# Kernel tuning notes

Measured on AMD Instinct MI355X. Metric: run time of the kernel, lower is better.

## Reference

```python
import jax, jax.numpy as jnp
import numpy as np


def setup_inputs() -> dict:
    key = jax.random.key(0)
    x = jax.random.normal(key, (8, 256, 16384), dtype=jnp.float32)
    gamma = jnp.zeros((1,), dtype=jnp.float32)
    return {"x": x, "gamma": gamma}


def reference(x, gamma):
    # x: (B, C, T)
    # energy[b, i, j] = sum_t x[b, i, t] * x[b, j, t]  -> (B, C, C)
    energy = jnp.einsum('bit,bjt->bij', x, x)
    # max-subtract trick: attention = softmax(max_j(energy) - energy)
    energy_new = jnp.max(energy, axis=-1, keepdims=True) - energy
    attention = jax.nn.softmax(energy_new, axis=-1)
    # out[b, i, t] = sum_j attention[b, i, j] * x[b, j, t]
    out = jnp.einsum('bij,bjt->bit', attention, x)
    return gamma * out + x
```

## Files before the change

### kernel.cpp

```cpp
#include <hip/hip_runtime.h>
#include <hip/hip_bf16.h>

#define NB 8
#define NC 256
#define NT 16384

using bf16x8 = __attribute__((ext_vector_type(8))) __bf16;
using f32x16 = __attribute__((ext_vector_type(16))) float;
using f32x4  = __attribute__((ext_vector_type(4))) float;
using u32x4  = __attribute__((ext_vector_type(4))) unsigned int;

__device__ __forceinline__ unsigned short bf16_rne(float f) {
  unsigned int u = __float_as_uint(f);
  u += 0x7FFFu + ((u >> 16) & 1u);
  return (unsigned short)(u >> 16);
}

__device__ __forceinline__ unsigned int pack_bf16_pair_rne(float f_lo, float f_hi) {
  unsigned int a = __float_as_uint(f_lo), b = __float_as_uint(f_hi);
  a += 0x7FFFu + ((a >> 16) & 1u);
  b += 0x7FFFu + ((b >> 16) & 1u);
  return __builtin_amdgcn_perm(b, a, 0x07060302u);
}

template <int ITERS>
__global__ __launch_bounds__(1024) void k_gram(const float* __restrict__ x,
                                               float* __restrict__ Gp) {
  __shared__ __align__(16) unsigned short lds[256 * 72];
  const int b   = blockIdx.y;
  const int kc  = blockIdx.x;
  const int tid = threadIdx.x;
  const int l   = tid & 63, w = tid >> 6;
  const int wr  = w >> 2, wc = w & 3;
  const int l31 = l & 31, lh = l >> 5;

  const float* __restrict__ xb = x + (size_t)b * NC * NT;

  const int sr = tid >> 2;
  const int sq = tid & 3;
  const float* sp = xb + (size_t)sr * NT + kc * (ITERS * 64) + sq * 16;

  f32x4 r0 = ((const f32x4*)sp)[0];
  f32x4 r1 = ((const f32x4*)sp)[1];
  f32x4 r2 = ((const f32x4*)sp)[2];
  f32x4 r3 = ((const f32x4*)sp)[3];

  f32x16 acc00, acc01, acc10, acc11;
#pragma unroll
  for (int i = 0; i < 16; ++i) { acc00[i] = 0.f; acc01[i] = 0.f; acc10[i] = 0.f; acc11[i] = 0.f; }

#pragma unroll 1
  for (int it = 0; it < ITERS; ++it) {
    __syncthreads();
    u32x4 p0, p1;
    p0[0] = pack_bf16_pair_rne(r0[0], r0[1]); p0[1] = pack_bf16_pair_rne(r0[2], r0[3]);
    p0[2] = pack_bf16_pair_rne(r1[0], r1[1]); p0[3] = pack_bf16_pair_rne(r1[2], r1[3]);
    p1[0] = pack_bf16_pair_rne(r2[0], r2[1]); p1[1] = pack_bf16_pair_rne(r2[2], r2[3]);
    p1[2] = pack_bf16_pair_rne(r3[0], r3[1]); p1[3] = pack_bf16_pair_rne(r3[2], r3[3]);
    u32x4* dst = (u32x4*)&lds[sr * 72 + sq * 16];
    dst[0] = p0;
    dst[1] = p1;
    if (it < ITERS - 1) {
      const float* np = sp + (it + 1) * 64;
      r0 = ((const f32x4*)np)[0]; r1 = ((const f32x4*)np)[1];
      r2 = ((const f32x4*)np)[2]; r3 = ((const f32x4*)np)[3];
    }
    __syncthreads();
#pragma unroll
    for (int s = 0; s < 4; ++s) {
      const int ko = s * 16 + lh * 8;
      bf16x8 a0 = *(const bf16x8*)&lds[(wr * 64 +      l31) * 72 + ko];
      bf16x8 a1 = *(const bf16x8*)&lds[(wr * 64 + 32 + l31) * 72 + ko];
      bf16x8 b0 = *(const bf16x8*)&lds[(wc * 64 +      l31) * 72 + ko];
      bf16x8 b1 = *(const bf16x8*)&lds[(wc * 64 + 32 + l31) * 72 + ko];
      acc00 = __builtin_amdgcn_mfma_f32_32x32x16_bf16(a0, b0, acc00, 0, 0, 0);
      acc01 = __builtin_amdgcn_mfma_f32_32x32x16_bf16(a0, b1, acc01, 0, 0, 0);
      acc10 = __builtin_amdgcn_mfma_f32_32x32x16_bf16(a1, b0, acc10, 0, 0, 0);
      acc11 = __builtin_amdgcn_mfma_f32_32x32x16_bf16(a1, b1, acc11, 0, 0, 0);
    }
  }

  float* __restrict__ Gb = Gp + ((size_t)kc * NB + b) * NC * NC;
  const int ibase = wr * 64 + 4 * lh;
  const int jbase = wc * 64 + l31;
#pragma unroll
  for (int g = 0; g < 16; ++g) {
    const int ir = (g & 3) + 8 * (g >> 2);
    Gb[(ibase + ir) * NC      + jbase     ] = acc00[g];
    Gb[(ibase + ir) * NC      + jbase + 32] = acc01[g];
    Gb[(ibase + 32 + ir) * NC + jbase     ] = acc10[g];
    Gb[(ibase + 32 + ir) * NC + jbase + 32] = acc11[g];
  }
}

template <int NKC>
__global__ __launch_bounds__(256) void k_softmax(const float* __restrict__ Gp,
                                                 const float* __restrict__ gamma,
                                                 unsigned short* __restrict__ Att) {
  const int row = blockIdx.x * 4 + (threadIdx.x >> 6);
  const int l   = threadIdx.x & 63;
  const int i   = row & (NC - 1);
  const float* base = Gp + (size_t)row * NC + l * 4;

  f32x4 v; v[0] = 0.f; v[1] = 0.f; v[2] = 0.f; v[3] = 0.f;
#pragma unroll
  for (int kc = 0; kc < NKC; ++kc) {
    f32x4 p = *(const f32x4*)(base + (size_t)kc * (NB * NC * NC));
    v[0] += p[0]; v[1] += p[1]; v[2] += p[2]; v[3] += p[3];
  }

  float mn = fminf(fminf(v[0], v[1]), fminf(v[2], v[3]));
#pragma unroll
  for (int m = 32; m >= 1; m >>= 1) mn = fminf(mn, __shfl_xor(mn, m, 64));
  float p0 = __expf(mn - v[0]), p1 = __expf(mn - v[1]);
  float p2 = __expf(mn - v[2]), p3 = __expf(mn - v[3]);
  float s = (p0 + p1) + (p2 + p3);
#pragma unroll
  for (int m = 32; m >= 1; m >>= 1) s += __shfl_xor(s, m, 64);
  const float sc = gamma[0] / s;

  const int j0 = 4 * l;
  ushort4 o;
  o.x = bf16_rne(p0 * sc + ((j0 + 0) == i ? 1.f : 0.f));
  o.y = bf16_rne(p1 * sc + ((j0 + 1) == i ? 1.f : 0.f));
  o.z = bf16_rne(p2 * sc + ((j0 + 2) == i ? 1.f : 0.f));
  o.w = bf16_rne(p3 * sc + ((j0 + 3) == i ? 1.f : 0.f));
  *(ushort4*)(Att + (size_t)row * NC + j0) = o;
}

__global__ __launch_bounds__(1024) void k_out(const float* __restrict__ x,
                                              const unsigned short* __restrict__ Att,
                                              float* __restrict__ y) {
  __shared__ __align__(16) float bs[32 * 260];
  __shared__ __align__(16) unsigned short as_[256 * 40];
  const int b   = blockIdx.y;
  const int t0  = blockIdx.x * 256;
  const int tid = threadIdx.x;
  const int l   = tid & 63, w = tid >> 6;
  const int rbw = w >> 3, cbw = w & 7;
  const int l31 = l & 31, lh = l >> 5;

  const float* __restrict__ xb = x + (size_t)b * NC * NT;
  const unsigned short* __restrict__ Ab = Att + (size_t)b * NC * NC;

  const int bk = tid >> 5, bf = tid & 31;
  const int ar = tid >> 2, aseg = tid & 3;

  const float* bsp = xb + (size_t)bk * NT + t0 + bf * 4;
  f32x4 rb0 = *(const f32x4*)bsp;
  f32x4 rb1 = *(const f32x4*)(bsp + 128);
  u32x4 ra  = *(const u32x4*)(Ab + ar * NC + aseg * 8);

  f32x16 acc0, acc1, acc2, acc3;
#pragma unroll
  for (int i = 0; i < 16; ++i) { acc0[i] = 0.f; acc1[i] = 0.f; acc2[i] = 0.f; acc3[i] = 0.f; }

#pragma unroll 1
  for (int it = 0; it < 8; ++it) {
    __syncthreads();
    *(f32x4*)&bs[bk * 260 + bf * 4]       = rb0;
    *(f32x4*)&bs[bk * 260 + 128 + bf * 4] = rb1;
    *(u32x4*)&as_[ar * 40 + aseg * 8]     = ra;
    if (it < 7) {
      const float* np = bsp + (size_t)(it + 1) * 32 * NT;
      rb0 = *(const f32x4*)np;
      rb1 = *(const f32x4*)(np + 128);
      ra  = *(const u32x4*)(Ab + ar * NC + (it + 1) * 32 + aseg * 8);
    }
    __syncthreads();
#pragma unroll
    for (int s = 0; s < 2; ++s) {
      const int kr = s * 16 + lh * 8;
      const int tc = cbw * 32 + l31;
      float f0 = bs[(kr + 0) * 260 + tc], f1 = bs[(kr + 1) * 260 + tc];
      float f2 = bs[(kr + 2) * 260 + tc], f3 = bs[(kr + 3) * 260 + tc];
      float f4 = bs[(kr + 4) * 260 + tc], f5 = bs[(kr + 5) * 260 + tc];
      float f6 = bs[(kr + 6) * 260 + tc], f7 = bs[(kr + 7) * 260 + tc];
      u32x4 pk;
      pk[0] = pack_bf16_pair_rne(f0, f1); pk[1] = pack_bf16_pair_rne(f2, f3);
      pk[2] = pack_bf16_pair_rne(f4, f5); pk[3] = pack_bf16_pair_rne(f6, f7);
      bf16x8 bfrag = __builtin_bit_cast(bf16x8, pk);
      const int ao = s * 16 + lh * 8;
      bf16x8 a0 = *(const bf16x8*)&as_[(rbw * 128 +      l31) * 40 + ao];
      bf16x8 a1 = *(const bf16x8*)&as_[(rbw * 128 + 32 + l31) * 40 + ao];
      bf16x8 a2 = *(const bf16x8*)&as_[(rbw * 128 + 64 + l31) * 40 + ao];
      bf16x8 a3 = *(const bf16x8*)&as_[(rbw * 128 + 96 + l31) * 40 + ao];
      acc0 = __builtin_amdgcn_mfma_f32_32x32x16_bf16(a0, bfrag, acc0, 0, 0, 0);
      acc1 = __builtin_amdgcn_mfma_f32_32x32x16_bf16(a1, bfrag, acc1, 0, 0, 0);
      acc2 = __builtin_amdgcn_mfma_f32_32x32x16_bf16(a2, bfrag, acc2, 0, 0, 0);
      acc3 = __builtin_amdgcn_mfma_f32_32x32x16_bf16(a3, bfrag, acc3, 0, 0, 0);
    }
  }

  const int tg = t0 + cbw * 32 + l31;
  const int ib = rbw * 128 + 4 * lh;
#pragma unroll
  for (int g = 0; g < 16; ++g) {
    const int ir = (g & 3) + 8 * (g >> 2);
    size_t i0 = (size_t)(b * NC + ib + ir) * NT + tg;
    y[i0] = acc0[g];
    y[i0 + (size_t)32 * NT] = acc1[g];
    y[i0 + (size_t)64 * NT] = acc2[g];
    y[i0 + (size_t)96 * NT] = acc3[g];
  }
}

extern "C" void kernel_launch(void* const* d_in, const int* in_sizes, int n_in,
                              void* d_out, int out_size, void* d_ws, size_t ws_size,
                              hipStream_t stream) {
  const float* x     = (const float*)d_in[0];
  const float* gamma = (const float*)d_in[1];
  float* y = (float*)d_out;

  const size_t chunk_bytes = (size_t)NB * NC * NC * sizeof(float);
  const size_t att_bytes   = (size_t)NB * NC * NC * sizeof(unsigned short);

  int nkc;
  if      (ws_size >= 32 * chunk_bytes + att_bytes) nkc = 32;
  else if (ws_size >= 16 * chunk_bytes + att_bytes) nkc = 16;
  else if (ws_size >=  8 * chunk_bytes + att_bytes) nkc = 8;
  else                                              nkc = 4;

  float* Gp = (float*)d_ws;
  unsigned short* Att = (unsigned short*)((char*)d_ws + (size_t)nkc * chunk_bytes);

  switch (nkc) {
    case 32:
      k_gram<8>  <<<dim3(32, NB), 1024, 0, stream>>>(x, Gp);
      k_softmax<32><<<dim3(NB * NC / 4), 256, 0, stream>>>(Gp, gamma, Att);
      break;
    case 16:
      k_gram<16> <<<dim3(16, NB), 1024, 0, stream>>>(x, Gp);
      k_softmax<16><<<dim3(NB * NC / 4), 256, 0, stream>>>(Gp, gamma, Att);
      break;
    case 8:
      k_gram<32> <<<dim3(8, NB), 1024, 0, stream>>>(x, Gp);
      k_softmax<8><<<dim3(NB * NC / 4), 256, 0, stream>>>(Gp, gamma, Att);
      break;
    default:
      k_gram<64> <<<dim3(4, NB), 1024, 0, stream>>>(x, Gp);
      k_softmax<4><<<dim3(NB * NC / 4), 256, 0, stream>>>(Gp, gamma, Att);
      break;
  }
  k_out<<<dim3(NT / 256, NB), 1024, 0, stream>>>(x, Att, y);
}
```

Before: 284.0 us.

## Load attention fragments directly from global, use lighter barriers and nontemporal output stores

The output kernel stops staging the bf16 attention matrix through LDS. Each wave now loads its A fragments straight from global memory, where they should hit in cache because the matrix is small and shared by every block. Both kernels replace __syncthreads with a raw s_barrier, and only the publishing barrier first waits for outstanding LDS operations, so in-flight global prefetches are no longer drained at the barriers. Output stores become nontemporal to avoid polluting the cache with the streamed result. The risks are global-load latency in the MFMA inner loop and the correctness of the hand-written barrier semantics.

```diff
diff --git a/kernel.cpp b/kernel.cpp
--- a/kernel.cpp
+++ b/kernel.cpp
@@ -21,6 +21,16 @@
   a += 0x7FFFu + ((a >> 16) & 1u);
   b += 0x7FFFu + ((b >> 16) & 1u);
   return __builtin_amdgcn_perm(b, a, 0x07060302u);
+}
+
+__device__ __forceinline__ void barrier_acq() {
+  __builtin_amdgcn_s_barrier();
+  asm volatile("" ::: "memory");
+}
+__device__ __forceinline__ void barrier_lds_pub() {
+  asm volatile("s_waitcnt lgkmcnt(0)" ::: "memory");
+  __builtin_amdgcn_s_barrier();
+  asm volatile("" ::: "memory");
 }
 
 template <int ITERS>
@@ -51,7 +61,7 @@
 
 #pragma unroll 1
   for (int it = 0; it < ITERS; ++it) {
-    __syncthreads();
+    barrier_acq();
     u32x4 p0, p1;
     p0[0] = pack_bf16_pair_rne(r0[0], r0[1]); p0[1] = pack_bf16_pair_rne(r0[2], r0[3]);
     p0[2] = pack_bf16_pair_rne(r1[0], r1[1]); p0[3] = pack_bf16_pair_rne(r1[2], r1[3]);
@@ -65,7 +75,7 @@
       r0 = ((const f32x4*)np)[0]; r1 = ((const f32x4*)np)[1];
       r2 = ((const f32x4*)np)[2]; r3 = ((const f32x4*)np)[3];
     }
-    __syncthreads();
+    barrier_lds_pub();
 #pragma unroll
     for (int s = 0; s < 4; ++s) {
       const int ko = s * 16 + lh * 8;
@@ -132,7 +142,6 @@
                                               const unsigned short* __restrict__ Att,
                                               float* __restrict__ y) {
   __shared__ __align__(16) float bs[32 * 260];
-  __shared__ __align__(16) unsigned short as_[256 * 40];
   const int b   = blockIdx.y;
   const int t0  = blockIdx.x * 256;
   const int tid = threadIdx.x;
@@ -144,12 +153,15 @@
   const unsigned short* __restrict__ Ab = Att + (size_t)b * NC * NC;
 
   const int bk = tid >> 5, bf = tid & 31;
-  const int ar = tid >> 2, aseg = tid & 3;
 
   const float* bsp = xb + (size_t)bk * NT + t0 + bf * 4;
   f32x4 rb0 = *(const f32x4*)bsp;
   f32x4 rb1 = *(const f32x4*)(bsp + 128);
-  u32x4 ra  = *(const u32x4*)(Ab + ar * NC + aseg * 8);
+
+  const unsigned short* a0p = Ab + (size_t)(rbw * 128 +      l31) * NC;
+  const unsigned short* a1p = Ab + (size_t)(rbw * 128 + 32 + l31) * NC;
+  const unsigned short* a2p = Ab + (size_t)(rbw * 128 + 64 + l31) * NC;
+  const unsigned short* a3p = Ab + (size_t)(rbw * 128 + 96 + l31) * NC;
 
   f32x16 acc0, acc1, acc2, acc3;
 #pragma unroll
@@ -157,17 +169,15 @@
 
 #pragma unroll 1
   for (int it = 0; it < 8; ++it) {
-    __syncthreads();
+    barrier_acq();
     *(f32x4*)&bs[bk * 260 + bf * 4]       = rb0;
     *(f32x4*)&bs[bk * 260 + 128 + bf * 4] = rb1;
-    *(u32x4*)&as_[ar * 40 + aseg * 8]     = ra;
     if (it < 7) {
       const float* np = bsp + (size_t)(it + 1) * 32 * NT;
       rb0 = *(const f32x4*)np;
       rb1 = *(const f32x4*)(np + 128);
-      ra  = *(const u32x4*)(Ab + ar * NC + (it + 1) * 32 + aseg * 8);
-    }
-    __syncthreads();
+    }
+    barrier_lds_pub();
 #pragma unroll
     for (int s = 0; s < 2; ++s) {
       const int kr = s * 16 + lh * 8;
@@ -180,11 +190,11 @@
       pk[0] = pack_bf16_pair_rne(f0, f1); pk[1] = pack_bf16_pair_rne(f2, f3);
       pk[2] = pack_bf16_pair_rne(f4, f5); pk[3] = pack_bf16_pair_rne(f6, f7);
       bf16x8 bfrag = __builtin_bit_cast(bf16x8, pk);
-      const int ao = s * 16 + lh * 8;
-      bf16x8 a0 = *(const bf16x8*)&as_[(rbw * 128 +      l31) * 40 + ao];
-      bf16x8 a1 = *(const bf16x8*)&as_[(rbw * 128 + 32 + l31) * 40 + ao];
-      bf16x8 a2 = *(const bf16x8*)&as_[(rbw * 128 + 64 + l31) * 40 + ao];
-      bf16x8 a3 = *(const bf16x8*)&as_[(rbw * 128 + 96 + l31) * 40 + ao];
+      const int ao = it * 32 + s * 16 + lh * 8;
+      bf16x8 a0 = *(const bf16x8*)(a0p + ao);
+      bf16x8 a1 = *(const bf16x8*)(a1p + ao);
+      bf16x8 a2 = *(const bf16x8*)(a2p + ao);
+      bf16x8 a3 = *(const bf16x8*)(a3p + ao);
       acc0 = __builtin_amdgcn_mfma_f32_32x32x16_bf16(a0, bfrag, acc0, 0, 0, 0);
       acc1 = __builtin_amdgcn_mfma_f32_32x32x16_bf16(a1, bfrag, acc1, 0, 0, 0);
       acc2 = __builtin_amdgcn_mfma_f32_32x32x16_bf16(a2, bfrag, acc2, 0, 0, 0);
@@ -198,10 +208,10 @@
   for (int g = 0; g < 16; ++g) {
     const int ir = (g & 3) + 8 * (g >> 2);
     size_t i0 = (size_t)(b * NC + ib + ir) * NT + tg;
-    y[i0] = acc0[g];
-    y[i0 + (size_t)32 * NT] = acc1[g];
-    y[i0 + (size_t)64 * NT] = acc2[g];
-    y[i0 + (size_t)96 * NT] = acc3[g];
+    __builtin_nontemporal_store(acc0[g], &y[i0]);
+    __builtin_nontemporal_store(acc1[g], &y[i0 + (size_t)32 * NT]);
+    __builtin_nontemporal_store(acc2[g], &y[i0 + (size_t)64 * NT]);
+    __builtin_nontemporal_store(acc3[g], &y[i0 + (size_t)96 * NT]);
   }
 }
 
```

Result: slower. 319.3 us (+12.4%).
